# Kernel tuning notes

Hardware: AMD Instinct MI355X
Metric: run time of the kernel (lower is better)

Reference implementation:

```python
import jax, jax.numpy as jnp
import numpy as np

N, T, B = 883, 12, 64
DIN, DOUT, CHEB_K, DE = 2, 64, 2, 10


def setup_inputs() -> dict:
    key = jax.random.key(0)
    ks = jax.random.split(key, 12)
    x = jax.random.normal(ks[0], (B, T, N, DIN), dtype=jnp.float32)
    adj = jax.random.uniform(ks[1], (N, N), dtype=jnp.float32) / N  # roughly row-stochastic
    node_embeddings = jax.random.normal(ks[2], (N, DE), dtype=jnp.float32)
    s = 0.05
    DI = DIN + DOUT
    # forward-direction cell pools (AGCRN-style)
    Wg_f = jax.random.normal(ks[3], (DE, CHEB_K, DI, 2 * DOUT), dtype=jnp.float32) * s
    bg_f = jax.random.normal(ks[4], (DE, 2 * DOUT), dtype=jnp.float32) * s
    Wc_f = jax.random.normal(ks[5], (DE, CHEB_K, DI, DOUT), dtype=jnp.float32) * s
    bc_f = jax.random.normal(ks[6], (DE, DOUT), dtype=jnp.float32) * s
    # backward-direction cell pools
    Wg_b = jax.random.normal(ks[7], (DE, CHEB_K, DI, 2 * DOUT), dtype=jnp.float32) * s
    bg_b = jax.random.normal(ks[8], (DE, 2 * DOUT), dtype=jnp.float32) * s
    Wc_b = jax.random.normal(ks[9], (DE, CHEB_K, DI, DOUT), dtype=jnp.float32) * s
    bc_b = jax.random.normal(ks[10], (DE, DOUT), dtype=jnp.float32) * s
    return {"x": x, "adj": adj, "node_embeddings": node_embeddings,
            "Wg_f": Wg_f, "bg_f": bg_f, "Wc_f": Wc_f, "bc_f": bc_f,
            "Wg_b": Wg_b, "bg_b": bg_b, "Wc_b": Wc_b, "bc_b": bc_b}


def _cheb_supports(adj, E):
    # adaptive adjacency from node embeddings (AGCRN) combined with given adj
    A = jax.nn.softmax(jax.nn.relu(E @ E.T), axis=1)
    S = A + adj
    polys = [jnp.eye(N, dtype=S.dtype), S]
    for _ in range(2, CHEB_K):
        polys.append(2.0 * S @ polys[-1] - polys[-2])
    return jnp.stack(polys[:CHEB_K])  # [K,N,N]


def _run_direction(x_seq, adj, E, Wg, bg, Wc, bc):
    supports = _cheb_supports(adj, E)                 # [K,N,N]
    Wg_n = jnp.einsum('nd,dkio->nkio', E, Wg)         # [N,K,DI,2*DOUT]
    bg_n = E @ bg                                     # [N,2*DOUT]
    Wc_n = jnp.einsum('nd,dkio->nkio', E, Wc)
    bc_n = E @ bc

    def gconv(inp, Wn, bn):
        xg = jnp.einsum('knm,bmi->bkni', supports, inp)
        return jnp.einsum('bkni,nkio->bno', xg, Wn) + bn

    def step(h, xt):
        inp = jnp.concatenate([xt, h], axis=-1)       # [B,N,DI]
        zr = jax.nn.sigmoid(gconv(inp, Wg_n, bg_n))
        z, r = jnp.split(zr, 2, axis=-1)
        inp2 = jnp.concatenate([xt, r * h], axis=-1)
        hc = jnp.tanh(gconv(inp2, Wc_n, bc_n))
        h_new = z * h + (1.0 - z) * hc
        return h_new, h_new

    h0 = jnp.zeros((x_seq.shape[0], N, DOUT), dtype=x_seq.dtype)
    _, hs = jax.lax.scan(step, h0, jnp.swapaxes(x_seq, 0, 1))  # [T,B,N,DOUT]
    return jnp.swapaxes(hs, 0, 1)                              # [B,T,N,DOUT]


def reference(x, adj, node_embeddings, Wg_f, bg_f, Wc_f, bc_f, Wg_b, bg_b, Wc_b, bc_b):
    out1 = _run_direction(x, adj, node_embeddings, Wg_f, bg_f, Wc_f, bc_f)
    out2 = _run_direction(jnp.flip(x, axis=1), adj, node_embeddings, Wg_b, bg_b, Wc_b, bc_b)
    # BiSTFGRN assigns out2 without re-flipping; stay faithful.
    return jnp.concatenate([out1, out2], axis=-1)  # [B,T,N,2*DOUT]
```

## Files before the change

kernel.cpp:

```cpp
#include <hip/hip_runtime.h>
#include <math.h>

#define N_NODES 883
#define KPAD 896
#define T_STEPS 12
#define DE 10
#define KI 132
#define NCOLS 8192
#define XCOLS 1536
#define WSTR 160
#define ASTR 168
#define GOSTR (128 * WSTR)
#define COSTR (64 * WSTR)

typedef _Float16 f16;
typedef __attribute__((ext_vector_type(2))) _Float16 f16x2;
typedef __attribute__((ext_vector_type(4))) _Float16 f16x4;
typedef __attribute__((ext_vector_type(8))) _Float16 f16x8;
typedef __attribute__((ext_vector_type(4))) float f32x4;

__device__ inline void gload16(const void* g, void* l) {
    __builtin_amdgcn_global_load_lds(
        (const __attribute__((address_space(1))) unsigned int*)g,
        (__attribute__((address_space(3))) unsigned int*)l, 16, 0, 0);
}

__global__ __launch_bounds__(256) void k_computeS(const float* __restrict__ E,
                                                  const float* __restrict__ adj,
                                                  f16* __restrict__ Sh) {
    int n = blockIdx.x;
    int tid = threadIdx.x;
    __shared__ float l[N_NODES];
    __shared__ float red[8];
    float En[DE];
#pragma unroll
    for (int d = 0; d < DE; ++d) En[d] = E[n * DE + d];

    float lmax = -1e30f;
    for (int m = tid; m < N_NODES; m += 256) {
        float dot = 0.f;
#pragma unroll
        for (int d = 0; d < DE; ++d) dot += En[d] * E[m * DE + d];
        dot = fmaxf(dot, 0.f);
        l[m] = dot;
        lmax = fmaxf(lmax, dot);
    }
    int wave = tid >> 6, lane = tid & 63;
    for (int off = 32; off > 0; off >>= 1) lmax = fmaxf(lmax, __shfl_down(lmax, off));
    if (lane == 0) red[wave] = lmax;
    __syncthreads();
    float gmax = fmaxf(fmaxf(red[0], red[1]), fmaxf(red[2], red[3]));
    __syncthreads();

    float lsum = 0.f;
    for (int m = tid; m < N_NODES; m += 256) {
        float e = expf(l[m] - gmax);
        l[m] = e;
        lsum += e;
    }
    for (int off = 32; off > 0; off >>= 1) lsum += __shfl_down(lsum, off);
    if (lane == 0) red[wave] = lsum;
    __syncthreads();
    float inv = 1.0f / (red[0] + red[1] + red[2] + red[3]);
    for (int m = tid; m < N_NODES; m += 256) {
        Sh[(size_t)n * KPAD + m] = (f16)(l[m] * inv + adj[(size_t)n * N_NODES + m]);
    }
}

__global__ void k_buildXT(const float* __restrict__ x, f16* __restrict__ XTt) {
    int idx = blockIdx.x * blockDim.x + threadIdx.x;
    if (idx >= XCOLS * N_NODES) return;
    int m = idx % N_NODES;
    int c = idx / N_NODES;
    int t = c >> 7;
    int b = (c >> 1) & 63;
    int i = c & 1;
    XTt[(size_t)c * KPAD + m] = (f16)x[(((size_t)b * T_STEPS + t) * N_NODES + m) * 2 + i];
}

__global__ void k_reorgW(const float* __restrict__ Wg_f, const float* __restrict__ Wg_b,
                         const float* __restrict__ Wc_f, const float* __restrict__ Wc_b,
                         float* __restrict__ Wg_r, float* __restrict__ Wc_r) {
    const int GTOT = 2 * DE * GOSTR;
    const int CTOT = 2 * DE * COSTR;
    int idx = blockIdx.x * blockDim.x + threadIdx.x;
    if (idx < GTOT) {
        int k = idx % WSTR;
        int o = (idx / WSTR) & 127;
        int d = (idx / GOSTR) % DE;
        int dir = idx / (DE * GOSTR);
        const float* W = dir ? Wg_b : Wg_f;
        float v = 0.f;
        if (k < KI) {
            int kc = k / 66, i = k % 66;
            v = W[(((size_t)d * 2 + kc) * 66 + i) * 128 + o];
        }
        Wg_r[idx] = v;
    } else if (idx < GTOT + CTOT) {
        int j = idx - GTOT;
        int k = j % WSTR;
        int o = (j / WSTR) & 63;
        int d = (j / COSTR) % DE;
        int dir = j / (DE * COSTR);
        const float* W = dir ? Wc_b : Wc_f;
        float v = 0.f;
        if (k < KI) {
            int kc = k / 66, i = k % 66;
            v = W[(((size_t)d * 2 + kc) * 66 + i) * 64 + o];
        }
        Wc_r[j] = v;
    }
}

__global__ __launch_bounds__(256) void k_buildW2(
    const float* __restrict__ E,
    const float* __restrict__ Wg_r, const float* __restrict__ Wc_r,
    f16* __restrict__ WgT, f16* __restrict__ WcT) {
    int grp = blockIdx.x, dir = blockIdx.y, z = blockIdx.z;
    int n0 = grp * 16;
    int tid = threadIdx.x;
    __shared__ float Es[16][DE];
    if (tid < 16 * DE) {
        int nn = tid / DE, d = tid % DE;
        int n = n0 + nn;
        Es[nn][d] = (n < N_NODES) ? E[n * DE + d] : 0.f;
    }
    __syncthreads();

    bool gate = z < 4;
    const float* src = gate ? (Wg_r + (size_t)dir * DE * GOSTR)
                            : (Wc_r + (size_t)dir * DE * COSTR);
    f16* dst = gate ? WgT : WcT;
    int ostr = gate ? GOSTR : COSTR;
    int slot0 = gate ? z * 1280 : (z - 4) * 1280;

#pragma unroll
    for (int it = 0; it < 5; ++it) {
        int f = (slot0 + it * 256 + tid) * 4;
        float4 v[DE];
#pragma unroll
        for (int d = 0; d < DE; ++d)
            v[d] = *(const float4*)&src[(size_t)d * ostr + f];
#pragma unroll
        for (int nn = 0; nn < 16; ++nn) {
            int n = n0 + nn;
            if (n >= N_NODES) break;
            float a0 = 0.f, a1 = 0.f, a2 = 0.f, a3 = 0.f;
#pragma unroll
            for (int d = 0; d < DE; ++d) {
                float e = Es[nn][d];
                a0 += e * v[d].x; a1 += e * v[d].y;
                a2 += e * v[d].z; a3 += e * v[d].w;
            }
            f16x4 r = {(f16)a0, (f16)a1, (f16)a2, (f16)a3};
            *(f16x4*)&dst[(size_t)(dir * N_NODES + n) * ostr + f] = r;
        }
    }
}

__global__ __launch_bounds__(128) void k_buildBias(
    const float* __restrict__ E,
    const float* __restrict__ bg_f, const float* __restrict__ bg_b,
    const float* __restrict__ bc_f, const float* __restrict__ bc_b,
    float* __restrict__ bgn, float* __restrict__ bcn) {
    int n = blockIdx.x, dir = blockIdx.y;
    int o = threadIdx.x;
    const float* bg = dir ? bg_b : bg_f;
    const float* bc = dir ? bc_b : bc_f;
    float Ed[DE];
#pragma unroll
    for (int d = 0; d < DE; ++d) Ed[d] = E[n * DE + d];
    float v = 0.f;
#pragma unroll
    for (int d = 0; d < DE; ++d) v += Ed[d] * bg[d * 128 + o];
    bgn[(size_t)(dir * N_NODES + n) * 128 + o] = v;
    if (o < 64) {
        float c = 0.f;
#pragma unroll
        for (int d = 0; d < DE; ++d) c += Ed[d] * bc[d * 64 + o];
        bcn[(size_t)(dir * N_NODES + n) * 64 + o] = c;
    }
}

__global__ __launch_bounds__(256) void k_transpose(const f16* __restrict__ V,
                                                   f16* __restrict__ VT) {
    __shared__ f16 tile[64][66];
    int c0 = blockIdx.x * 64;
    int n0 = blockIdx.y * 64;
    int tid = threadIdx.x;
#pragma unroll
    for (int it = 0; it < 2; ++it) {
        int chunk = tid + it * 256;
        int r = chunk >> 3, g = chunk & 7;
        int n = n0 + r;
        f16 tmp[8];
        if (n < N_NODES) {
            f16x8 v = *(const f16x8*)&V[(size_t)n * NCOLS + c0 + g * 8];
#pragma unroll
            for (int j = 0; j < 8; ++j) tmp[j] = v[j];
        } else {
#pragma unroll
            for (int j = 0; j < 8; ++j) tmp[j] = (f16)0.f;
        }
#pragma unroll
        for (int j = 0; j < 8; ++j) tile[g * 8 + j][r] = tmp[j];
    }
    __syncthreads();
#pragma unroll
    for (int it = 0; it < 2; ++it) {
        int chunk = tid + it * 256;
        int cc = chunk >> 3, m = chunk & 7;
        f16x8 v;
#pragma unroll
        for (int j = 0; j < 8; ++j) v[j] = tile[cc][m * 8 + j];
        *(f16x8*)&VT[(size_t)(c0 + cc) * KPAD + n0 + m * 8] = v;
    }
}

__global__ __launch_bounds__(256) void k_gemm_f16(const f16* __restrict__ A,
                                                  const f16* __restrict__ Bt,
                                                  f16* __restrict__ C, int NC) {
    __shared__ f16 Als[128 * 32];
    __shared__ f16 Bls[128 * 32];
    int tid = threadIdx.x;
    int w = tid >> 6, l = tid & 63;
    int wr = w >> 1, wc = w & 1;
    int row0 = blockIdx.y * 128;
    int col0 = blockIdx.x * 128;
    int rr = l >> 2;
    int cc = (l & 3) * 8;
    int lr = l & 15, lg = l >> 4;

    const f16* a0 = A + (size_t)(row0 + w * 32 + rr) * KPAD + cc;
    const f16* a1 = a0 + (size_t)16 * KPAD;
    const f16* b0 = Bt + (size_t)(col0 + w * 32 + rr) * KPAD + cc;
    const f16* b1 = b0 + (size_t)16 * KPAD;
    f16* la0 = &Als[(w * 32) * 32];
    f16* la1 = &Als[(w * 32 + 16) * 32];
    f16* lb0 = &Bls[(w * 32) * 32];
    f16* lb1 = &Bls[(w * 32 + 16) * 32];

    f32x4 acc[4][4];
#pragma unroll
    for (int m = 0; m < 4; ++m)
#pragma unroll
        for (int n = 0; n < 4; ++n) acc[m][n] = (f32x4)(0.f);

    for (int kt = 0; kt < KPAD / 32; ++kt) {
        int k0 = kt * 32;
        gload16(a0 + k0, la0);
        gload16(a1 + k0, la1);
        gload16(b0 + k0, lb0);
        gload16(b1 + k0, lb1);
        __syncthreads();
        f16x8 af[4], bf[4];
#pragma unroll
        for (int m = 0; m < 4; ++m)
            af[m] = *(const f16x8*)&Als[(wr * 64 + m * 16 + lr) * 32 + lg * 8];
#pragma unroll
        for (int n = 0; n < 4; ++n)
            bf[n] = *(const f16x8*)&Bls[(wc * 64 + n * 16 + lr) * 32 + lg * 8];
#pragma unroll
        for (int m = 0; m < 4; ++m)
#pragma unroll
            for (int n = 0; n < 4; ++n)
                acc[m][n] = __builtin_amdgcn_mfma_f32_16x16x32_f16(af[m], bf[n], acc[m][n], 0, 0, 0);
        __syncthreads();
    }

#pragma unroll
    for (int m = 0; m < 4; ++m) {
        int gr0 = row0 + wr * 64 + m * 16 + lg * 4;
#pragma unroll
        for (int n = 0; n < 4; ++n) {
            int gc = col0 + wc * 64 + n * 16 + lr;
            f32x4 v = acc[m][n];
#pragma unroll
            for (int q = 0; q < 4; ++q) {
                int r = gr0 + q;
                if (r < N_NODES) C[(size_t)r * NC + gc] = (f16)v[q];
            }
        }
    }
}

__global__ __launch_bounds__(256) void k_apply_gate(
    const float* __restrict__ x, const float* __restrict__ H,
    const f16* __restrict__ SXh, const f16* __restrict__ SHh,
    const f16* __restrict__ WgT, const float* __restrict__ bgn,
    f16* __restrict__ Zh, f16* __restrict__ RHh, int t) {
    int n = blockIdx.x, dir = blockIdx.y;
    int tid = threadIdx.x;
    int tt = dir ? (T_STEPS - 1 - t) : t;
    __shared__ f16 inpA[64 * ASTR];

    const float* hrow = H + (size_t)n * NCOLS + dir * 4096;
    const f16* shrow = SHh + (size_t)n * NCOLS + dir * 4096;

#pragma unroll
    for (int it = 0; it < 4; ++it) {
        int i4 = tid + it * 256;
        int b = i4 >> 4, j0 = (i4 & 15) * 4;
        float4 v = *(const float4*)&hrow[b * 64 + j0];
        f16x2 p0 = {(f16)v.x, (f16)v.y};
        f16x2 p1 = {(f16)v.z, (f16)v.w};
        *(f16x2*)&inpA[b * ASTR + 2 + j0] = p0;
        *(f16x2*)&inpA[b * ASTR + 4 + j0] = p1;
    }
#pragma unroll
    for (int it = 0; it < 8; ++it) {
        int i2 = tid + it * 256;
        int b = i2 >> 5, jp = i2 & 31;
        *(unsigned*)&inpA[b * ASTR + 68 + 2 * jp] = *(const unsigned*)&shrow[b * 64 + 2 * jp];
    }
    if (tid < 128) {
        int b = tid >> 1, i = tid & 1;
        inpA[b * ASTR + i] = (f16)x[(((size_t)b * T_STEPS + tt) * N_NODES + n) * 2 + i];
        inpA[b * ASTR + 66 + i] = SXh[(size_t)n * XCOLS + tt * 128 + b * 2 + i];
    }
    for (int idx = tid; idx < 64 * 14; idx += 256) {
        int b = idx / 14, p = idx % 14;
        *(unsigned*)&inpA[b * ASTR + 132 + 2 * p] = 0u;
    }
    __syncthreads();

    int w = tid >> 6, l = tid & 63;
    int lr = l & 15, lg = l >> 4;
    int o0 = w * 32;
    const f16* wbase = WgT + (size_t)(dir * N_NODES + n) * GOSTR;

    f32x4 acc[4][2];
#pragma unroll
    for (int m = 0; m < 4; ++m)
#pragma unroll
        for (int j = 0; j < 2; ++j) acc[m][j] = (f32x4)(0.f);

#pragma unroll
    for (int kt = 0; kt < 5; ++kt) {
        int k0 = kt * 32 + lg * 8;
        f16x8 af[4], bf[2];
#pragma unroll
        for (int m = 0; m < 4; ++m)
            af[m] = *(const f16x8*)&inpA[(m * 16 + lr) * ASTR + k0];
#pragma unroll
        for (int j = 0; j < 2; ++j)
            bf[j] = *(const f16x8*)&wbase[(size_t)(o0 + j * 16 + lr) * WSTR + k0];
#pragma unroll
        for (int m = 0; m < 4; ++m)
#pragma unroll
            for (int j = 0; j < 2; ++j)
                acc[m][j] = __builtin_amdgcn_mfma_f32_16x16x32_f16(af[m], bf[j], acc[m][j], 0, 0, 0);
    }

    const float* bias = bgn + (size_t)(dir * N_NODES + n) * 128;
    f16* zrow = Zh + (size_t)(dir * N_NODES + n) * 4096;
    f16* rhrow = RHh + (size_t)n * NCOLS + dir * 4096;
#pragma unroll
    for (int j = 0; j < 2; ++j) {
        int o = o0 + j * 16 + lr;
        float bo = bias[o];
        if (o < 64) {
#pragma unroll
            for (int m = 0; m < 4; ++m) {
                int b0 = m * 16 + lg * 4;
                f32x4 v = acc[m][j];
#pragma unroll
                for (int q = 0; q < 4; ++q)
                    zrow[(b0 + q) * 64 + o] = (f16)(1.f / (1.f + expf(-(v[q] + bo))));
            }
        } else {
            int jj = o - 64;
#pragma unroll
            for (int m = 0; m < 4; ++m) {
                int b0 = m * 16 + lg * 4;
                f32x4 v = acc[m][j];
#pragma unroll
                for (int q = 0; q < 4; ++q) {
                    float r = 1.f / (1.f + expf(-(v[q] + bo)));
                    rhrow[(b0 + q) * 64 + jj] = (f16)(r * hrow[(b0 + q) * 64 + jj]);
                }
            }
        }
    }
}

__global__ __launch_bounds__(256) void k_apply_cand(
    const float* __restrict__ x, const f16* __restrict__ SXh,
    const f16* __restrict__ SRHh, const f16* __restrict__ RHh,
    const f16* __restrict__ WcT, const float* __restrict__ bcn,
    const f16* __restrict__ Zh, float* __restrict__ H,
    f16* __restrict__ Hh, float* __restrict__ out, int t) {
    int n = blockIdx.x, dir = blockIdx.y;
    int tid = threadIdx.x;
    int tt = dir ? (T_STEPS - 1 - t) : t;
    __shared__ f16 inpA[64 * ASTR];

    const f16* rhrow = RHh + (size_t)n * NCOLS + dir * 4096;
    const f16* srhrow = SRHh + (size_t)n * NCOLS + dir * 4096;

#pragma unroll
    for (int it = 0; it < 8; ++it) {
        int i2 = tid + it * 256;
        int b = i2 >> 5, jp = i2 & 31;
        *(unsigned*)&inpA[b * ASTR + 2 + 2 * jp] = *(const unsigned*)&rhrow[b * 64 + 2 * jp];
        *(unsigned*)&inpA[b * ASTR + 68 + 2 * jp] = *(const unsigned*)&srhrow[b * 64 + 2 * jp];
    }
    if (tid < 128) {
        int b = tid >> 1, i = tid & 1;
        inpA[b * ASTR + i] = (f16)x[(((size_t)b * T_STEPS + tt) * N_NODES + n) * 2 + i];
        inpA[b * ASTR + 66 + i] = SXh[(size_t)n * XCOLS + tt * 128 + b * 2 + i];
    }
    for (int idx = tid; idx < 64 * 14; idx += 256) {
        int b = idx / 14, p = idx % 14;
        *(unsigned*)&inpA[b * ASTR + 132 + 2 * p] = 0u;
    }
    __syncthreads();

    int w = tid >> 6, l = tid & 63;
    int lr = l & 15, lg = l >> 4;
    const f16* wbase = WcT + (size_t)(dir * N_NODES + n) * COSTR;

    f32x4 acc[4];
#pragma unroll
    for (int j = 0; j < 4; ++j) acc[j] = (f32x4)(0.f);

#pragma unroll
    for (int kt = 0; kt < 5; ++kt) {
        int k0 = kt * 32 + lg * 8;
        f16x8 af = *(const f16x8*)&inpA[(w * 16 + lr) * ASTR + k0];
        f16x8 bf[4];
#pragma unroll
        for (int j = 0; j < 4; ++j)
            bf[j] = *(const f16x8*)&wbase[(size_t)(j * 16 + lr) * WSTR + k0];
#pragma unroll
        for (int j = 0; j < 4; ++j)
            acc[j] = __builtin_amdgcn_mfma_f32_16x16x32_f16(af, bf[j], acc[j], 0, 0, 0);
    }

    const float* bias = bcn + (size_t)(dir * N_NODES + n) * 64;
    const f16* zrow = Zh + (size_t)(dir * N_NODES + n) * 4096;
    float* hrow = H + (size_t)n * NCOLS + dir * 4096;
    f16* hhrow = Hh + (size_t)n * NCOLS + dir * 4096;
#pragma unroll
    for (int j = 0; j < 4; ++j) {
        int o = j * 16 + lr;
        float bo = bias[o];
        f32x4 v = acc[j];
#pragma unroll
        for (int q = 0; q < 4; ++q) {
            int b = w * 16 + lg * 4 + q;
            float hc = tanhf(v[q] + bo);
            float zv = (float)zrow[b * 64 + o];
            float hp = hrow[b * 64 + o];
            float hn = zv * hp + (1.f - zv) * hc;
            hrow[b * 64 + o] = hn;
            hhrow[b * 64 + o] = (f16)hn;
            out[(((size_t)b * T_STEPS + t) * N_NODES + n) * 128 + dir * 64 + o] = hn;
        }
    }
}

extern "C" void kernel_launch(void* const* d_in, const int* in_sizes, int n_in,
                              void* d_out, int out_size, void* d_ws, size_t ws_size,
                              hipStream_t stream) {
    const float* x    = (const float*)d_in[0];
    const float* adj  = (const float*)d_in[1];
    const float* E    = (const float*)d_in[2];
    const float* Wg_f = (const float*)d_in[3];
    const float* bg_f = (const float*)d_in[4];
    const float* Wc_f = (const float*)d_in[5];
    const float* bc_f = (const float*)d_in[6];
    const float* Wg_b = (const float*)d_in[7];
    const float* bg_b = (const float*)d_in[8];
    const float* Wc_b = (const float*)d_in[9];
    const float* bc_b = (const float*)d_in[10];
    float* out = (float*)d_out;

    size_t off = 0;
    auto alloc = [&](size_t bytes) {
        void* p = (char*)d_ws + off;
        off += (bytes + 255) & ~(size_t)255;
        return p;
    };
    f16*   Sh   = (f16*)alloc((size_t)KPAD * KPAD * 2);
    f16*   XTt  = (f16*)alloc((size_t)XCOLS * KPAD * 2);
    f16*   SXh  = (f16*)alloc((size_t)N_NODES * XCOLS * 2);
    float* H    = (float*)alloc((size_t)N_NODES * NCOLS * 4);
    f16*   Hh   = (f16*)alloc((size_t)N_NODES * NCOLS * 2);
    f16*   SHh  = (f16*)alloc((size_t)N_NODES * NCOLS * 2);
    f16*   RHh  = (f16*)alloc((size_t)N_NODES * NCOLS * 2);
    f16*   Zh   = (f16*)alloc((size_t)N_NODES * NCOLS * 2);
    f16*   HBt  = (f16*)alloc((size_t)NCOLS * KPAD * 2);
    f16*   RHBt = (f16*)alloc((size_t)NCOLS * KPAD * 2);
    f16*   WgT  = (f16*)alloc((size_t)2 * N_NODES * GOSTR * 2);
    f16*   WcT  = (f16*)alloc((size_t)2 * N_NODES * COSTR * 2);
    float* bgn  = (float*)alloc((size_t)2 * N_NODES * 128 * 4);
    float* bcn  = (float*)alloc((size_t)2 * N_NODES * 64 * 4);
    float* Wg_r = (float*)RHBt;
    float* Wc_r = Wg_r + (size_t)2 * DE * GOSTR;

    hipMemsetAsync(Sh, 0, (size_t)KPAD * KPAD * 2, stream);
    hipMemsetAsync(XTt, 0, (size_t)XCOLS * KPAD * 2, stream);
    hipMemsetAsync(H, 0, (size_t)N_NODES * NCOLS * 4, stream);
    hipMemsetAsync(SHh, 0, (size_t)N_NODES * NCOLS * 2, stream);

    k_computeS<<<N_NODES, 256, 0, stream>>>(E, adj, Sh);
    {
        int total = XCOLS * N_NODES;
        k_buildXT<<<(total + 255) / 256, 256, 0, stream>>>(x, XTt);
    }
    {
        int total = 2 * DE * (GOSTR + COSTR);
        k_reorgW<<<(total + 255) / 256, 256, 0, stream>>>(Wg_f, Wg_b, Wc_f, Wc_b, Wg_r, Wc_r);
    }
    k_buildW2<<<dim3(56, 2, 6), 256, 0, stream>>>(E, Wg_r, Wc_r, WgT, WcT);
    dim3 gnode(N_NODES, 2);
    k_buildBias<<<gnode, 128, 0, stream>>>(E, bg_f, bg_b, bc_f, bc_b, bgn, bcn);
    k_gemm_f16<<<dim3(XCOLS / 128, 7), 256, 0, stream>>>(Sh, XTt, SXh, XCOLS);

    dim3 gmain(NCOLS / 128, 7);
    dim3 gtr(NCOLS / 64, KPAD / 64);
    for (int t = 0; t < T_STEPS; ++t) {
        if (t > 0)
            k_gemm_f16<<<gmain, 256, 0, stream>>>(Sh, HBt, SHh, NCOLS);
        k_apply_gate<<<gnode, 256, 0, stream>>>(x, H, SXh, SHh, WgT, bgn,
                                                Zh, RHh, t);
        k_transpose<<<gtr, 256, 0, stream>>>(RHh, RHBt);
        k_gemm_f16<<<gmain, 256, 0, stream>>>(Sh, RHBt, SHh, NCOLS);
        k_apply_cand<<<gnode, 256, 0, stream>>>(x, SXh, SHh, RHh, WcT, bcn,
                                                Zh, H, Hh, out, t);
        k_transpose<<<gtr, 256, 0, stream>>>(Hh, HBt);
    }
}
```

Before: 1.786 ms.

## Fold bias into weight padding column and drop fp32 hidden state buffer

The node-specific bias is folded into the padded K slot of the per-node weights, and a constant 1.0 is written into the matching input column, so the MFMA adds the bias itself. This removes the bias kernel and the per-element bias loads. The fp32 hidden-state array is removed and both recurrent kernels read and write only the fp16 copy, which roughly halves hidden-state traffic. The recurrence now carries h in fp16 between steps, which can accumulate extra rounding error over the 12 steps.

```diff
diff --git a/kernel.cpp b/kernel.cpp
--- a/kernel.cpp
+++ b/kernel.cpp
@@ -80,6 +80,8 @@
 
 __global__ void k_reorgW(const float* __restrict__ Wg_f, const float* __restrict__ Wg_b,
                          const float* __restrict__ Wc_f, const float* __restrict__ Wc_b,
+                         const float* __restrict__ bg_f, const float* __restrict__ bg_b,
+                         const float* __restrict__ bc_f, const float* __restrict__ bc_b,
                          float* __restrict__ Wg_r, float* __restrict__ Wc_r) {
     const int GTOT = 2 * DE * GOSTR;
     const int CTOT = 2 * DE * COSTR;
@@ -89,11 +91,13 @@
         int o = (idx / WSTR) & 127;
         int d = (idx / GOSTR) % DE;
         int dir = idx / (DE * GOSTR);
-        const float* W = dir ? Wg_b : Wg_f;
         float v = 0.f;
         if (k < KI) {
+            const float* W = dir ? Wg_b : Wg_f;
             int kc = k / 66, i = k % 66;
             v = W[(((size_t)d * 2 + kc) * 66 + i) * 128 + o];
+        } else if (k == KI) {
+            v = (dir ? bg_b : bg_f)[d * 128 + o];
         }
         Wg_r[idx] = v;
     } else if (idx < GTOT + CTOT) {
@@ -102,11 +106,13 @@
         int o = (j / WSTR) & 63;
         int d = (j / COSTR) % DE;
         int dir = j / (DE * COSTR);
-        const float* W = dir ? Wc_b : Wc_f;
         float v = 0.f;
         if (k < KI) {
+            const float* W = dir ? Wc_b : Wc_f;
             int kc = k / 66, i = k % 66;
             v = W[(((size_t)d * 2 + kc) * 66 + i) * 64 + o];
+        } else if (k == KI) {
+            v = (dir ? bc_b : bc_f)[d * 64 + o];
         }
         Wc_r[j] = v;
     }
@@ -155,30 +161,6 @@
             f16x4 r = {(f16)a0, (f16)a1, (f16)a2, (f16)a3};
             *(f16x4*)&dst[(size_t)(dir * N_NODES + n) * ostr + f] = r;
         }
-    }
-}
-
-__global__ __launch_bounds__(128) void k_buildBias(
-    const float* __restrict__ E,
-    const float* __restrict__ bg_f, const float* __restrict__ bg_b,
-    const float* __restrict__ bc_f, const float* __restrict__ bc_b,
-    float* __restrict__ bgn, float* __restrict__ bcn) {
-    int n = blockIdx.x, dir = blockIdx.y;
-    int o = threadIdx.x;
-    const float* bg = dir ? bg_b : bg_f;
-    const float* bc = dir ? bc_b : bc_f;
-    float Ed[DE];
-#pragma unroll
-    for (int d = 0; d < DE; ++d) Ed[d] = E[n * DE + d];
-    float v = 0.f;
-#pragma unroll
-    for (int d = 0; d < DE; ++d) v += Ed[d] * bg[d * 128 + o];
-    bgn[(size_t)(dir * N_NODES + n) * 128 + o] = v;
-    if (o < 64) {
-        float c = 0.f;
-#pragma unroll
-        for (int d = 0; d < DE; ++d) c += Ed[d] * bc[d * 64 + o];
-        bcn[(size_t)(dir * N_NODES + n) * 64 + o] = c;
     }
 }
 
@@ -285,33 +267,25 @@
 }
 
 __global__ __launch_bounds__(256) void k_apply_gate(
-    const float* __restrict__ x, const float* __restrict__ H,
+    const float* __restrict__ x, const f16* __restrict__ Hh,
     const f16* __restrict__ SXh, const f16* __restrict__ SHh,
-    const f16* __restrict__ WgT, const float* __restrict__ bgn,
-    f16* __restrict__ Zh, f16* __restrict__ RHh, int t) {
+    const f16* __restrict__ WgT,
+    f16* __restrict__ Zh, f16* __restrict__ RHh, int t, int first) {
     int n = blockIdx.x, dir = blockIdx.y;
     int tid = threadIdx.x;
     int tt = dir ? (T_STEPS - 1 - t) : t;
     __shared__ f16 inpA[64 * ASTR];
 
-    const float* hrow = H + (size_t)n * NCOLS + dir * 4096;
+    const f16* hhrow = Hh + (size_t)n * NCOLS + dir * 4096;
     const f16* shrow = SHh + (size_t)n * NCOLS + dir * 4096;
 
-#pragma unroll
-    for (int it = 0; it < 4; ++it) {
-        int i4 = tid + it * 256;
-        int b = i4 >> 4, j0 = (i4 & 15) * 4;
-        float4 v = *(const float4*)&hrow[b * 64 + j0];
-        f16x2 p0 = {(f16)v.x, (f16)v.y};
-        f16x2 p1 = {(f16)v.z, (f16)v.w};
-        *(f16x2*)&inpA[b * ASTR + 2 + j0] = p0;
-        *(f16x2*)&inpA[b * ASTR + 4 + j0] = p1;
-    }
 #pragma unroll
     for (int it = 0; it < 8; ++it) {
         int i2 = tid + it * 256;
         int b = i2 >> 5, jp = i2 & 31;
-        *(unsigned*)&inpA[b * ASTR + 68 + 2 * jp] = *(const unsigned*)&shrow[b * 64 + 2 * jp];
+        *(unsigned*)&inpA[b * ASTR + 2 + 2 * jp] = *(const unsigned*)&hhrow[b * 64 + 2 * jp];
+        *(unsigned*)&inpA[b * ASTR + 68 + 2 * jp] =
+            first ? 0u : *(const unsigned*)&shrow[b * 64 + 2 * jp];
     }
     if (tid < 128) {
         int b = tid >> 1, i = tid & 1;
@@ -320,7 +294,7 @@
     }
     for (int idx = tid; idx < 64 * 14; idx += 256) {
         int b = idx / 14, p = idx % 14;
-        *(unsigned*)&inpA[b * ASTR + 132 + 2 * p] = 0u;
+        *(unsigned*)&inpA[b * ASTR + 132 + 2 * p] = (p == 0) ? 0x00003C00u : 0u;
     }
     __syncthreads();
 
@@ -352,13 +326,11 @@
                 acc[m][j] = __builtin_amdgcn_mfma_f32_16x16x32_f16(af[m], bf[j], acc[m][j], 0, 0, 0);
     }
 
-    const float* bias = bgn + (size_t)(dir * N_NODES + n) * 128;
     f16* zrow = Zh + (size_t)(dir * N_NODES + n) * 4096;
     f16* rhrow = RHh + (size_t)n * NCOLS + dir * 4096;
 #pragma unroll
     for (int j = 0; j < 2; ++j) {
         int o = o0 + j * 16 + lr;
-        float bo = bias[o];
         if (o < 64) {
 #pragma unroll
             for (int m = 0; m < 4; ++m) {
@@ -366,7 +338,7 @@
                 f32x4 v = acc[m][j];
 #pragma unroll
                 for (int q = 0; q < 4; ++q)
-                    zrow[(b0 + q) * 64 + o] = (f16)(1.f / (1.f + expf(-(v[q] + bo))));
+                    zrow[(b0 + q) * 64 + o] = (f16)(1.f / (1.f + expf(-v[q])));
             }
         } else {
             int jj = o - 64;
@@ -376,8 +348,9 @@
                 f32x4 v = acc[m][j];
 #pragma unroll
                 for (int q = 0; q < 4; ++q) {
-                    float r = 1.f / (1.f + expf(-(v[q] + bo)));
-                    rhrow[(b0 + q) * 64 + jj] = (f16)(r * hrow[(b0 + q) * 64 + jj]);
+                    float r = 1.f / (1.f + expf(-v[q]));
+                    rhrow[(b0 + q) * 64 + jj] =
+                        (f16)(r * (float)hhrow[(b0 + q) * 64 + jj]);
                 }
             }
         }
@@ -387,8 +360,7 @@
 __global__ __launch_bounds__(256) void k_apply_cand(
     const float* __restrict__ x, const f16* __restrict__ SXh,
     const f16* __restrict__ SRHh, const f16* __restrict__ RHh,
-    const f16* __restrict__ WcT, const float* __restrict__ bcn,
-    const f16* __restrict__ Zh, float* __restrict__ H,
+    const f16* __restrict__ WcT, const f16* __restrict__ Zh,
     f16* __restrict__ Hh, float* __restrict__ out, int t) {
     int n = blockIdx.x, dir = blockIdx.y;
     int tid = threadIdx.x;
@@ -412,7 +384,7 @@
     }
     for (int idx = tid; idx < 64 * 14; idx += 256) {
         int b = idx / 14, p = idx % 14;
-        *(unsigned*)&inpA[b * ASTR + 132 + 2 * p] = 0u;
+        *(unsigned*)&inpA[b * ASTR + 132 + 2 * p] = (p == 0) ? 0x00003C00u : 0u;
     }
     __syncthreads();
 
@@ -437,23 +409,19 @@
             acc[j] = __builtin_amdgcn_mfma_f32_16x16x32_f16(af, bf[j], acc[j], 0, 0, 0);
     }
 
-    const float* bias = bcn + (size_t)(dir * N_NODES + n) * 64;
     const f16* zrow = Zh + (size_t)(dir * N_NODES + n) * 4096;
-    float* hrow = H + (size_t)n * NCOLS + dir * 4096;
     f16* hhrow = Hh + (size_t)n * NCOLS + dir * 4096;
 #pragma unroll
     for (int j = 0; j < 4; ++j) {
         int o = j * 16 + lr;
-        float bo = bias[o];
         f32x4 v = acc[j];
 #pragma unroll
         for (int q = 0; q < 4; ++q) {
             int b = w * 16 + lg * 4 + q;
-            float hc = tanhf(v[q] + bo);
+            float hc = tanhf(v[q]);
             float zv = (float)zrow[b * 64 + o];
-            float hp = hrow[b * 64 + o];
+            float hp = (float)hhrow[b * 64 + o];
             float hn = zv * hp + (1.f - zv) * hc;
-            hrow[b * 64 + o] = hn;
             hhrow[b * 64 + o] = (f16)hn;
             out[(((size_t)b * T_STEPS + t) * N_NODES + n) * 128 + dir * 64 + o] = hn;
         }
@@ -485,7 +453,6 @@
     f16*   Sh   = (f16*)alloc((size_t)KPAD * KPAD * 2);
     f16*   XTt  = (f16*)alloc((size_t)XCOLS * KPAD * 2);
     f16*   SXh  = (f16*)alloc((size_t)N_NODES * XCOLS * 2);
-    float* H    = (float*)alloc((size_t)N_NODES * NCOLS * 4);
     f16*   Hh   = (f16*)alloc((size_t)N_NODES * NCOLS * 2);
     f16*   SHh  = (f16*)alloc((size_t)N_NODES * NCOLS * 2);
     f16*   RHh  = (f16*)alloc((size_t)N_NODES * NCOLS * 2);
@@ -494,15 +461,12 @@
     f16*   RHBt = (f16*)alloc((size_t)NCOLS * KPAD * 2);
     f16*   WgT  = (f16*)alloc((size_t)2 * N_NODES * GOSTR * 2);
     f16*   WcT  = (f16*)alloc((size_t)2 * N_NODES * COSTR * 2);
-    float* bgn  = (float*)alloc((size_t)2 * N_NODES * 128 * 4);
-    float* bcn  = (float*)alloc((size_t)2 * N_NODES * 64 * 4);
     float* Wg_r = (float*)RHBt;
     float* Wc_r = Wg_r + (size_t)2 * DE * GOSTR;
 
     hipMemsetAsync(Sh, 0, (size_t)KPAD * KPAD * 2, stream);
     hipMemsetAsync(XTt, 0, (size_t)XCOLS * KPAD * 2, stream);
-    hipMemsetAsync(H, 0, (size_t)N_NODES * NCOLS * 4, stream);
-    hipMemsetAsync(SHh, 0, (size_t)N_NODES * NCOLS * 2, stream);
+    hipMemsetAsync(Hh, 0, (size_t)N_NODES * NCOLS * 2, stream);
 
     k_computeS<<<N_NODES, 256, 0, stream>>>(E, adj, Sh);
     {
@@ -511,24 +475,25 @@
     }
     {
         int total = 2 * DE * (GOSTR + COSTR);
-        k_reorgW<<<(total + 255) / 256, 256, 0, stream>>>(Wg_f, Wg_b, Wc_f, Wc_b, Wg_r, Wc_r);
+        k_reorgW<<<(total + 255) / 256, 256, 0, stream>>>(Wg_f, Wg_b, Wc_f, Wc_b,
+                                                          bg_f, bg_b, bc_f, bc_b,
+                                                          Wg_r, Wc_r);
     }
     k_buildW2<<<dim3(56, 2, 6), 256, 0, stream>>>(E, Wg_r, Wc_r, WgT, WcT);
+    k_gemm_f16<<<dim3(XCOLS / 128, 7), 256, 0, stream>>>(Sh, XTt, SXh, XCOLS);
+
     dim3 gnode(N_NODES, 2);
-    k_buildBias<<<gnode, 128, 0, stream>>>(E, bg_f, bg_b, bc_f, bc_b, bgn, bcn);
-    k_gemm_f16<<<dim3(XCOLS / 128, 7), 256, 0, stream>>>(Sh, XTt, SXh, XCOLS);
-
     dim3 gmain(NCOLS / 128, 7);
     dim3 gtr(NCOLS / 64, KPAD / 64);
     for (int t = 0; t < T_STEPS; ++t) {
         if (t > 0)
             k_gemm_f16<<<gmain, 256, 0, stream>>>(Sh, HBt, SHh, NCOLS);
-        k_apply_gate<<<gnode, 256, 0, stream>>>(x, H, SXh, SHh, WgT, bgn,
-                                                Zh, RHh, t);
+        k_apply_gate<<<gnode, 256, 0, stream>>>(x, Hh, SXh, SHh, WgT,
+                                                Zh, RHh, t, t == 0 ? 1 : 0);
         k_transpose<<<gtr, 256, 0, stream>>>(RHh, RHBt);
         k_gemm_f16<<<gmain, 256, 0, stream>>>(Sh, RHBt, SHh, NCOLS);
-        k_apply_cand<<<gnode, 256, 0, stream>>>(x, SXh, SHh, RHh, WcT, bcn,
-                                                Zh, H, Hh, out, t);
+        k_apply_cand<<<gnode, 256, 0, stream>>>(x, SXh, SHh, RHh, WcT,
+                                                Zh, Hh, out, t);
         k_transpose<<<gtr, 256, 0, stream>>>(Hh, HBt);
     }
 }
```

After: 1.574 ms. 1.13x faster.
